# Kernel optimization log

Hardware: AMD Instinct MI355X
Metric: run time of the kernel (lower is better)

The kernel has to match this reference:

```python
import jax, jax.numpy as jnp
import numpy as np

N = 20000
E = 640000
IN_DIM = 128
HID = 128
OUT = 64


def setup_inputs() -> dict:
    key = jax.random.key(0)
    ks = jax.random.split(key, 16)
    s = 0.05
    inp = {
        'feat': jax.random.normal(ks[0], (N, IN_DIM), jnp.float32),
        'edge_index': jax.random.randint(ks[1], (2, E), 0, N, jnp.int64),
        # GCNConv params
        'W_gcn': jax.random.normal(ks[2], (IN_DIM, HID), jnp.float32) * s,
        'b_gcn': jnp.zeros((HID,), jnp.float32),
        # SAGEConv params (lin_l: aggregated neighbors w/ bias; lin_r: root, no bias)
        'W_sage_l': jax.random.normal(ks[3], (HID, HID), jnp.float32) * s,
        'b_sage_l': jnp.zeros((HID,), jnp.float32),
        'W_sage_r': jax.random.normal(ks[4], (HID, HID), jnp.float32) * s,
        # policy MLP
        'W1': jax.random.normal(ks[5], (HID, HID), jnp.float32) * s,
        'b1': jnp.zeros((HID,), jnp.float32),
        'W2': jax.random.normal(ks[6], (HID, HID), jnp.float32) * s,
        'b2': jnp.zeros((HID,), jnp.float32),
        'W3': jax.random.normal(ks[7], (HID, OUT), jnp.float32) * s,
        'b3': jnp.zeros((OUT,), jnp.float32),
        # value head
        'Wv': jax.random.normal(ks[8], (HID, 1), jnp.float32) * s,
        'bv': jnp.zeros((1,), jnp.float32),
    }
    return inp


def _gcn(feat, src, dst, W, b):
    # PyG GCNConv: add self loops, sym-normalize by deg^-1/2 on both ends
    loop = jnp.arange(N, dtype=src.dtype)
    s = jnp.concatenate([src, loop])
    d = jnp.concatenate([dst, loop])
    deg = jax.ops.segment_sum(jnp.ones_like(d, jnp.float32), d, num_segments=N)
    dinv = jnp.where(deg > 0, jax.lax.rsqrt(deg), 0.0)
    x = feat @ W  # [N, HID]
    msg = x[s] * (dinv[s] * dinv[d])[:, None]  # [E+N, HID]
    return jax.ops.segment_sum(msg, d, num_segments=N) + b


def _sage_mean(h, src, dst, Wl, bl, Wr):
    # PyG SAGEConv(aggr='mean'): lin_l(mean_neigh) + lin_r(root)
    neigh_sum = jax.ops.segment_sum(h[src], dst, num_segments=N)
    cnt = jax.ops.segment_sum(jnp.ones_like(dst, jnp.float32), dst, num_segments=N)
    mean = neigh_sum / jnp.maximum(cnt, 1.0)[:, None]
    return mean @ Wl + bl + h @ Wr


def reference(feat, edge_index, W_gcn, b_gcn, W_sage_l, b_sage_l, W_sage_r,
              W1, b1, W2, b2, W3, b3, Wv, bv):
    src, dst = edge_index[0], edge_index[1]
    h = jax.nn.relu(_gcn(feat, src, dst, W_gcn, b_gcn))
    h = jax.nn.relu(_sage_mean(h, src, dst, W_sage_l, b_sage_l, W_sage_r))
    # policy MLP (GELU exact, matching torch nn.GELU default)
    z = jax.nn.gelu(h @ W1 + b1, approximate=False)
    z = jax.nn.gelu(z @ W2 + b2, approximate=False)
    means = z @ W3 + b3  # [N, OUT]
    values = (h @ Wv + bv)[:, 0]  # [N]
    return (means, values)
```

## Files before the change

### kernel.cpp

```cpp
#include <hip/hip_runtime.h>
#include <math.h>


typedef __attribute__((ext_vector_type(8))) short short8;
typedef __attribute__((ext_vector_type(4))) float floatx4;

__device__ __forceinline__ unsigned short f2b(float f) {
    unsigned u = __float_as_uint(f);
    unsigned r = (u + 0x7fffu + ((u >> 16) & 1u)) >> 16;
    return (unsigned short)r;
}
__device__ __forceinline__ float b2f_lo(unsigned v) {
    return __uint_as_float(v << 16);
}
__device__ __forceinline__ float b2f_hi(unsigned v) {
    return __uint_as_float(v & 0xffff0000u);
}
__device__ __forceinline__ floatx4 MFMA(short8 a, short8 b, floatx4 c) {
    return __builtin_amdgcn_mfma_f32_16x16x32_bf16(a, b, c, 0, 0, 0);
}
__device__ __forceinline__ float gelu_exact(float x) {
    return 0.5f * x * (1.0f + erff(x * 0.70710678118654752440f));
}

#define FRAG(P, ct, ks, lane) (*(const short8*)((P) + (((((ct)*4 + (ks))*64) + (lane)) << 3)))


__global__ __launch_bounds__(256) void count_pack_kernel(
    const int* __restrict__ eidx, int E, int* __restrict__ cnt,
    const float* Wg, const float* Wsl, const float* Wsr,
    const float* W1, const float* W2, const float* W3,
    unsigned short* Pg, unsigned short* Psl, unsigned short* Psr,
    unsigned short* P1, unsigned short* P2, unsigned short* P3,
    int countBlocks)
{
    if ((int)blockIdx.x < countBlocks) {
        int e = blockIdx.x * 256 + threadIdx.x;
        if (e < E) atomicAdd(&cnt[eidx[E + e]], 1);
        return;
    }
    int t = (blockIdx.x - countBlocks) * 256 + threadIdx.x;
    const float* W; unsigned short* P; int NC = 128; int base;
    if (t < 2048)       { W = Wg;  P = Pg;  base = t; }
    else if (t < 4096)  { W = Wsl; P = Psl; base = t - 2048; }
    else if (t < 6144)  { W = Wsr; P = Psr; base = t - 4096; }
    else if (t < 8192)  { W = W1;  P = P1;  base = t - 6144; }
    else if (t < 10240) { W = W2;  P = P2;  base = t - 8192; }
    else if (t < 11264) { W = W3;  P = P3;  base = t - 10240; NC = 64; }
    else return;
    int l  = base & 63;
    int ks = (base >> 6) & 3;
    int ct = base >> 8;
    int n  = ct * 16 + (l & 15);
    int k0 = ks * 32 + ((l >> 4) << 3);
    short8 v;
    #pragma unroll
    for (int j = 0; j < 8; j++) v[j] = (short)f2b(W[(size_t)(k0 + j) * NC + n]);
    *(short8*)(P + ((size_t)base << 3)) = v;
}


__global__ __launch_bounds__(256) void scan_kernel(
    const int* __restrict__ cnt, int N,
    int* __restrict__ row_ptr, int* __restrict__ wptr, float* __restrict__ dinv,
    int* __restrict__ gflags, int* __restrict__ gsums)
{
    __shared__ int sh[256];
    __shared__ int s_off;
    int b = blockIdx.x, tid = threadIdx.x;
    int i0 = b * 1024 + tid * 4;
    int v0 = (i0 + 0 < N) ? cnt[i0 + 0] : 0;
    int v1 = (i0 + 1 < N) ? cnt[i0 + 1] : 0;
    int v2 = (i0 + 2 < N) ? cnt[i0 + 2] : 0;
    int v3 = (i0 + 3 < N) ? cnt[i0 + 3] : 0;
    int tot = v0 + v1 + v2 + v3;
    sh[tid] = tot;
    __syncthreads();
    for (int off = 1; off < 256; off <<= 1) {
        int t = (tid >= off) ? sh[tid - off] : 0;
        __syncthreads();
        sh[tid] += t;
        __syncthreads();
    }
    if (tid == 255) {
        gsums[b] = sh[255];
        __hip_atomic_store(&gflags[b], 1, __ATOMIC_RELEASE, __HIP_MEMORY_SCOPE_AGENT);
    }
    if (tid == 0) {
        int off = 0;
        for (int j = 0; j < b; j++) {
            while (__hip_atomic_load(&gflags[j], __ATOMIC_ACQUIRE,
                                     __HIP_MEMORY_SCOPE_AGENT) == 0) {}
            off += gsums[j];
        }
        s_off = off;
    }
    __syncthreads();
    int excl = s_off + sh[tid] - tot;
    if (i0 + 0 < N) { row_ptr[i0 + 0] = excl;                wptr[i0 + 0] = excl;                dinv[i0 + 0] = rsqrtf((float)(v0 + 1)); }
    if (i0 + 1 < N) { row_ptr[i0 + 1] = excl + v0;           wptr[i0 + 1] = excl + v0;           dinv[i0 + 1] = rsqrtf((float)(v1 + 1)); }
    if (i0 + 2 < N) { row_ptr[i0 + 2] = excl + v0 + v1;      wptr[i0 + 2] = excl + v0 + v1;      dinv[i0 + 2] = rsqrtf((float)(v2 + 1)); }
    if (i0 + 3 < N) { row_ptr[i0 + 3] = excl + v0 + v1 + v2; wptr[i0 + 3] = excl + v0 + v1 + v2; dinv[i0 + 3] = rsqrtf((float)(v3 + 1)); }
    if (b == (int)gridDim.x - 1 && tid == 255) row_ptr[N] = s_off + sh[255];
}


__global__ __launch_bounds__(256) void fill_gemm_kernel(
    const int* __restrict__ eidx, int E, int N,
    int* __restrict__ wptr, int* __restrict__ col,
    const float* __restrict__ feat, const float* __restrict__ dinv,
    const unsigned short* __restrict__ Pg, unsigned short* __restrict__ xs,
    int M, int fillBlocks, int PS)
{
    if ((int)blockIdx.x < fillBlocks) {
        int p = blockIdx.x & 7;
        int chunk = blockIdx.x >> 3;
        int dlo = p * PS;
        int dhi = dlo + PS; if (dhi > N) dhi = N;
        #pragma unroll
        for (int it = 0; it < 8; it++) {
            int e = (chunk * 8 + it) * 256 + threadIdx.x;
            if (e < E) {
                int d = eidx[E + e];
                if (d >= dlo && d < dhi) {
                    int pos = atomicAdd(&wptr[d], 1);
                    col[pos] = eidx[e];
                }
            }
        }
        return;
    }
    int bid = blockIdx.x - fillBlocks;
    int w = bid * 4 + (threadIdx.x >> 6);
    if (w >= (M / 16) * 2) return;
    int lane = threadIdx.x & 63;
    int m = lane & 15, quad = lane >> 4;
    int rt = w >> 1, ch = w & 1;
    const float* arow = feat + (size_t)(rt * 16 + m) * 128;
    short8 a[4];
    #pragma unroll
    for (int ks = 0; ks < 4; ks++) {
        float4 f0 = *(const float4*)(arow + ks * 32 + quad * 8);
        float4 f1 = *(const float4*)(arow + ks * 32 + quad * 8 + 4);
        short8 s;
        s[0] = (short)f2b(f0.x); s[1] = (short)f2b(f0.y);
        s[2] = (short)f2b(f0.z); s[3] = (short)f2b(f0.w);
        s[4] = (short)f2b(f1.x); s[5] = (short)f2b(f1.y);
        s[6] = (short)f2b(f1.z); s[7] = (short)f2b(f1.w);
        a[ks] = s;
    }
    float dvr[4];
    #pragma unroll
    for (int reg = 0; reg < 4; reg++) dvr[reg] = dinv[rt * 16 + quad * 4 + reg];
    #pragma unroll
    for (int ct = 0; ct < 4; ct++) {
        floatx4 acc = {0.f, 0.f, 0.f, 0.f};
        #pragma unroll
        for (int ks = 0; ks < 4; ks++)
            acc = MFMA(a[ks], FRAG(Pg, ch * 4 + ct, ks, lane), acc);
        #pragma unroll
        for (int reg = 0; reg < 4; reg++)
            xs[(size_t)(rt * 16 + quad * 4 + reg) * 128 + (ch * 4 + ct) * 16 + m] =
                f2b(acc[reg] * dvr[reg]);
    }
}


#define ACCUM(q)                                   \
    acc[0] += b2f_lo((q).x); acc[1] += b2f_hi((q).x); \
    acc[2] += b2f_lo((q).y); acc[3] += b2f_hi((q).y); \
    acc[4] += b2f_lo((q).z); acc[5] += b2f_hi((q).z); \
    acc[6] += b2f_lo((q).w); acc[7] += b2f_hi((q).w);

template<bool GCN>
__global__ __launch_bounds__(256) void agg_kernel(
    const unsigned short* __restrict__ X, const int* __restrict__ row_ptr,
    const int* __restrict__ col, const float* __restrict__ dinv,
    const float* __restrict__ bias, unsigned short* __restrict__ Y, int N)
{
    int w = (int)((blockIdx.x * 256 + threadIdx.x) >> 6);
    if (w >= N) return;
    int lane = threadIdx.x & 63;
    int g = lane >> 4, t = lane & 15;
    const uint4* Xq = (const uint4*)X;
    int beg = row_ptr[w], end = row_ptr[w + 1];
    int deg = end - beg;

    float acc[8] = {0.f, 0.f, 0.f, 0.f, 0.f, 0.f, 0.f, 0.f};
    int jb = beg;
    for (; jb + 16 <= end; jb += 16) {
        int s0 = col[jb + g];
        int s1 = col[jb + g + 4];
        int s2 = col[jb + g + 8];
        int s3 = col[jb + g + 12];
        uint4 q0 = Xq[(size_t)s0 * 16 + t];
        uint4 q1 = Xq[(size_t)s1 * 16 + t];
        uint4 q2 = Xq[(size_t)s2 * 16 + t];
        uint4 q3 = Xq[(size_t)s3 * 16 + t];
        ACCUM(q0) ACCUM(q1) ACCUM(q2) ACCUM(q3)
    }
    for (; jb < end; jb += 4) {
        int j = jb + g;
        if (j < end) {
            int s = col[j];
            uint4 q = Xq[(size_t)s * 16 + t];
            ACCUM(q)
        }
    }
    #pragma unroll
    for (int i = 0; i < 8; i++) {
        acc[i] += __shfl_xor(acc[i], 16);
        acc[i] += __shfl_xor(acc[i], 32);
    }
    if (g == 0) {
        float out[8];
        if (GCN) {
            uint4 q = Xq[(size_t)w * 16 + t];
            ACCUM(q)
            float dw = dinv[w];
            float4 b0 = *(const float4*)(bias + t * 8);
            float4 b1 = *(const float4*)(bias + t * 8 + 4);
            out[0] = fmaxf(fmaf(acc[0], dw, b0.x), 0.f);
            out[1] = fmaxf(fmaf(acc[1], dw, b0.y), 0.f);
            out[2] = fmaxf(fmaf(acc[2], dw, b0.z), 0.f);
            out[3] = fmaxf(fmaf(acc[3], dw, b0.w), 0.f);
            out[4] = fmaxf(fmaf(acc[4], dw, b1.x), 0.f);
            out[5] = fmaxf(fmaf(acc[5], dw, b1.y), 0.f);
            out[6] = fmaxf(fmaf(acc[6], dw, b1.z), 0.f);
            out[7] = fmaxf(fmaf(acc[7], dw, b1.w), 0.f);
        } else {
            float rc = 1.0f / (float)(deg > 0 ? deg : 1);
            #pragma unroll
            for (int i = 0; i < 8; i++) out[i] = acc[i] * rc;
        }
        uint4 r;
        r.x = (unsigned)f2b(out[0]) | ((unsigned)f2b(out[1]) << 16);
        r.y = (unsigned)f2b(out[2]) | ((unsigned)f2b(out[3]) << 16);
        r.z = (unsigned)f2b(out[4]) | ((unsigned)f2b(out[5]) << 16);
        r.w = (unsigned)f2b(out[6]) | ((unsigned)f2b(out[7]) << 16);
        ((uint4*)Y)[(size_t)w * 16 + t] = r;
    }
}


__global__ __launch_bounds__(256) void sage_mlp_kernel(
    const unsigned short* __restrict__ mean, const unsigned short* __restrict__ h1,
    const unsigned short* __restrict__ Psl, const unsigned short* __restrict__ Psr,
    const float* __restrict__ bsl,
    const unsigned short* __restrict__ P1, const float* __restrict__ b1,
    const unsigned short* __restrict__ P2, const float* __restrict__ b2,
    const unsigned short* __restrict__ P3, const float* __restrict__ b3,
    const float* __restrict__ Wv, const float* __restrict__ bv,
    float* __restrict__ means, float* __restrict__ values, int M)
{
    __shared__ unsigned short z[4][16 * 136];
    int widx = threadIdx.x >> 6, lane = threadIdx.x & 63;
    int w = blockIdx.x * 4 + widx;
    if (w >= M / 16) return;
    int m = lane & 15, quad = lane >> 4;
    unsigned short* zt = &z[widx][0];
    int r0 = w * 16;

    short8 am[4], ar[4];
    #pragma unroll
    for (int ks = 0; ks < 4; ks++) {
        am[ks] = *(const short8*)(mean + (size_t)(r0 + m) * 128 + ks * 32 + quad * 8);
        ar[ks] = *(const short8*)(h1   + (size_t)(r0 + m) * 128 + ks * 32 + quad * 8);
    }

    float vpart[4] = {0.f, 0.f, 0.f, 0.f};
    #pragma unroll
    for (int ct = 0; ct < 8; ct++) {
        floatx4 acc = {0.f, 0.f, 0.f, 0.f};
        #pragma unroll
        for (int ks = 0; ks < 4; ks++) acc = MFMA(am[ks], FRAG(Psl, ct, ks, lane), acc);
        #pragma unroll
        for (int ks = 0; ks < 4; ks++) acc = MFMA(ar[ks], FRAG(Psr, ct, ks, lane), acc);
        float bb = bsl[ct * 16 + m];
        float wv = Wv[ct * 16 + m];
        #pragma unroll
        for (int reg = 0; reg < 4; reg++) {
            float o = fmaxf(acc[reg] + bb, 0.f);
            vpart[reg] = fmaf(o, wv, vpart[reg]);
            zt[(quad * 4 + reg) * 136 + ct * 16 + m] = f2b(o);
        }
    }
    #pragma unroll
    for (int off = 1; off <= 8; off <<= 1) {
        #pragma unroll
        for (int reg = 0; reg < 4; reg++)
            vpart[reg] += __shfl_xor(vpart[reg], off);
    }
    if (m == 0) {
        float bvv = bv[0];
        #pragma unroll
        for (int reg = 0; reg < 4; reg++)
            values[r0 + quad * 4 + reg] = vpart[reg] + bvv;
    }

    short8 a1[4];
    #pragma unroll
    for (int ks = 0; ks < 4; ks++)
        a1[ks] = *(const short8*)(zt + m * 136 + ks * 32 + quad * 8);

    #pragma unroll
    for (int ct = 0; ct < 8; ct++) {
        floatx4 acc = {0.f, 0.f, 0.f, 0.f};
        #pragma unroll
        for (int ks = 0; ks < 4; ks++) acc = MFMA(a1[ks], FRAG(P1, ct, ks, lane), acc);
        float bb = b1[ct * 16 + m];
        #pragma unroll
        for (int reg = 0; reg < 4; reg++)
            zt[(quad * 4 + reg) * 136 + ct * 16 + m] = f2b(gelu_exact(acc[reg] + bb));
    }
    short8 a2[4];
    #pragma unroll
    for (int ks = 0; ks < 4; ks++)
        a2[ks] = *(const short8*)(zt + m * 136 + ks * 32 + quad * 8);

    #pragma unroll
    for (int ct = 0; ct < 8; ct++) {
        floatx4 acc = {0.f, 0.f, 0.f, 0.f};
        #pragma unroll
        for (int ks = 0; ks < 4; ks++) acc = MFMA(a2[ks], FRAG(P2, ct, ks, lane), acc);
        float bb = b2[ct * 16 + m];
        #pragma unroll
        for (int reg = 0; reg < 4; reg++)
            zt[(quad * 4 + reg) * 136 + ct * 16 + m] = f2b(gelu_exact(acc[reg] + bb));
    }
    short8 a3[4];
    #pragma unroll
    for (int ks = 0; ks < 4; ks++)
        a3[ks] = *(const short8*)(zt + m * 136 + ks * 32 + quad * 8);

    #pragma unroll
    for (int ct = 0; ct < 4; ct++) {
        floatx4 acc = {0.f, 0.f, 0.f, 0.f};
        #pragma unroll
        for (int ks = 0; ks < 4; ks++) acc = MFMA(a3[ks], FRAG(P3, ct, ks, lane), acc);
        float bb = b3[ct * 16 + m];
        #pragma unroll
        for (int reg = 0; reg < 4; reg++)
            means[(size_t)(r0 + quad * 4 + reg) * 64 + ct * 16 + m] = acc[reg] + bb;
    }
}


extern "C" void kernel_launch(void* const* d_in, const int* in_sizes, int n_in,
                              void* d_out, int out_size, void* d_ws, size_t ws_size,
                              hipStream_t stream) {
    const float* feat  = (const float*)d_in[0];
    const int*   eidx  = (const int*)d_in[1];
    const float* W_gcn = (const float*)d_in[2];
    const float* b_gcn = (const float*)d_in[3];
    const float* W_sl  = (const float*)d_in[4];
    const float* b_sl  = (const float*)d_in[5];
    const float* W_sr  = (const float*)d_in[6];
    const float* W1    = (const float*)d_in[7];
    const float* b1    = (const float*)d_in[8];
    const float* W2    = (const float*)d_in[9];
    const float* b2    = (const float*)d_in[10];
    const float* W3    = (const float*)d_in[11];
    const float* b3    = (const float*)d_in[12];
    const float* Wv    = (const float*)d_in[13];
    const float* bv    = (const float*)d_in[14];

    const int N = in_sizes[0] / 128;
    const int E = in_sizes[1] / 2;

    char* ws = (char*)d_ws;
    size_t off = 0;
    auto alloc = [&](size_t bytes) -> void* {
        void* p = ws + off;
        off += (bytes + 255) & ~(size_t)255;
        return p;
    };
    int*   gflags  = (int*)alloc((size_t)(64 + N) * 4);
    int*   cnt     = gflags + 64;
    size_t zbytes  = (size_t)(64 + N) * 4;
    int*   gsums   = (int*)alloc(64 * 4);
    int*   row_ptr = (int*)alloc((size_t)(N + 1) * 4);
    int*   wptr    = (int*)alloc((size_t)N * 4);
    float* dinv    = (float*)alloc((size_t)N * 4);
    int*   col     = (int*)alloc((size_t)E * 4);
    unsigned short* xs   = (unsigned short*)alloc((size_t)N * 128 * 2);
    unsigned short* h1   = (unsigned short*)alloc((size_t)N * 128 * 2);
    unsigned short* mean = (unsigned short*)alloc((size_t)N * 128 * 2);
    unsigned short* Pg   = (unsigned short*)alloc(2048 * 8 * 2);
    unsigned short* Psl  = (unsigned short*)alloc(2048 * 8 * 2);
    unsigned short* Psr  = (unsigned short*)alloc(2048 * 8 * 2);
    unsigned short* P1   = (unsigned short*)alloc(2048 * 8 * 2);
    unsigned short* P2   = (unsigned short*)alloc(2048 * 8 * 2);
    unsigned short* P3   = (unsigned short*)alloc(1024 * 8 * 2);

    hipMemsetAsync(gflags, 0, zbytes, stream);

    const int countBlocks = (E + 255) / 256;
    const int packBlocks  = (11264 + 255) / 256;
    count_pack_kernel<<<countBlocks + packBlocks, 256, 0, stream>>>(
        eidx, E, cnt, W_gcn, W_sl, W_sr, W1, W2, W3,
        Pg, Psl, Psr, P1, P2, P3, countBlocks);

    const int NB = (N + 1023) / 1024;
    scan_kernel<<<NB, 256, 0, stream>>>(cnt, N, row_ptr, wptr, dinv, gflags, gsums);

    const int PS = (N + 7) / 8;
    const int chunks = (E + 2047) / 2048;
    const int fillBlocks = chunks * 8;
    const int gemmBlocks = ((N / 16) * 2 + 3) / 4;
    fill_gemm_kernel<<<fillBlocks + gemmBlocks, 256, 0, stream>>>(
        eidx, E, N, wptr, col, feat, dinv, Pg, xs, N, fillBlocks, PS);

    const int agrid = (N + 3) / 4;
    agg_kernel<true><<<agrid, 256, 0, stream>>>(xs, row_ptr, col, dinv, b_gcn, h1, N);
    agg_kernel<false><<<agrid, 256, 0, stream>>>(h1, row_ptr, col, dinv, nullptr, mean, N);

    sage_mlp_kernel<<<(N / 16 + 3) / 4, 256, 0, stream>>>(
        mean, h1, Psl, Psr, b_sl, P1, b1, P2, b2, P3, b3, Wv, bv,
        (float*)d_out, (float*)d_out + (size_t)N * 64, N);
}
```

Measured before the change: 221.0 us.

## Fuse all GNN stages into one persistent kernel with grid barriers

Replaces the five separate kernels (count/pack, scan, fill+GEMM, two aggregations, SAGE+MLP) with a single persistent mega-kernel of 240 blocks of 512 threads that moves between phases through atomic grid-wide barriers. CSR fill now appears to use a per-edge rank array instead of a partitioned atomic cursor. The aggregation also processes two destination rows per wave at once to raise memory-level parallelism. This removes kernel launch gaps and tail effects. In exchange it relies on all blocks being co-resident for the spin barriers, and it caps parallelism at a fixed grid.

```diff
diff --git a/kernel.cpp b/kernel.cpp
--- a/kernel.cpp
+++ b/kernel.cpp
@@ -7,47 +7,36 @@
 
 __device__ __forceinline__ unsigned short f2b(float f) {
     unsigned u = __float_as_uint(f);
-    unsigned r = (u + 0x7fffu + ((u >> 16) & 1u)) >> 16;
-    return (unsigned short)r;
-}
-__device__ __forceinline__ float b2f_lo(unsigned v) {
-    return __uint_as_float(v << 16);
-}
-__device__ __forceinline__ float b2f_hi(unsigned v) {
-    return __uint_as_float(v & 0xffff0000u);
-}
+    return (unsigned short)((u + 0x7fffu + ((u >> 16) & 1u)) >> 16);
+}
+__device__ __forceinline__ unsigned pack2(float a, float b) {
+    return (unsigned)f2b(a) | ((unsigned)f2b(b) << 16);
+}
+__device__ __forceinline__ float b2f_lo(unsigned v) { return __uint_as_float(v << 16); }
+__device__ __forceinline__ float b2f_hi(unsigned v) { return __uint_as_float(v & 0xffff0000u); }
 __device__ __forceinline__ floatx4 MFMA(short8 a, short8 b, floatx4 c) {
     return __builtin_amdgcn_mfma_f32_16x16x32_bf16(a, b, c, 0, 0, 0);
 }
 __device__ __forceinline__ float gelu_exact(float x) {
     return 0.5f * x * (1.0f + erff(x * 0.70710678118654752440f));
 }
-
 #define FRAG(P, ct, ks, lane) (*(const short8*)((P) + (((((ct)*4 + (ks))*64) + (lane)) << 3)))
 
-
-__global__ __launch_bounds__(256) void count_pack_kernel(
-    const int* __restrict__ eidx, int E, int* __restrict__ cnt,
-    const float* Wg, const float* Wsl, const float* Wsr,
-    const float* W1, const float* W2, const float* W3,
-    unsigned short* Pg, unsigned short* Psl, unsigned short* Psr,
-    unsigned short* P1, unsigned short* P2, unsigned short* P3,
-    int countBlocks)
-{
-    if ((int)blockIdx.x < countBlocks) {
-        int e = blockIdx.x * 256 + threadIdx.x;
-        if (e < E) atomicAdd(&cnt[eidx[E + e]], 1);
-        return;
-    }
-    int t = (blockIdx.x - countBlocks) * 256 + threadIdx.x;
-    const float* W; unsigned short* P; int NC = 128; int base;
-    if (t < 2048)       { W = Wg;  P = Pg;  base = t; }
-    else if (t < 4096)  { W = Wsl; P = Psl; base = t - 2048; }
-    else if (t < 6144)  { W = Wsr; P = Psr; base = t - 4096; }
-    else if (t < 8192)  { W = W1;  P = P1;  base = t - 6144; }
-    else if (t < 10240) { W = W2;  P = P2;  base = t - 8192; }
-    else if (t < 11264) { W = W3;  P = P3;  base = t - 10240; NC = 64; }
-    else return;
+__device__ __forceinline__ void gbar(int* bar, int slot, int nblk) {
+    __syncthreads();
+    if (threadIdx.x == 0) {
+        __threadfence();
+        __hip_atomic_fetch_add(&bar[slot * 32], 1, __ATOMIC_RELEASE,
+                               __HIP_MEMORY_SCOPE_AGENT);
+        while (__hip_atomic_load(&bar[slot * 32], __ATOMIC_ACQUIRE,
+                                 __HIP_MEMORY_SCOPE_AGENT) < nblk) {
+            __builtin_amdgcn_s_sleep(1);
+        }
+    }
+    __syncthreads();
+}
+
+__device__ __forceinline__ void pack_one(const float* W, unsigned short* P, int NC, int base) {
     int l  = base & 63;
     int ks = (base >> 6) & 3;
     int ct = base >> 8;
@@ -59,289 +48,300 @@
     *(short8*)(P + ((size_t)base << 3)) = v;
 }
 
-
-__global__ __launch_bounds__(256) void scan_kernel(
-    const int* __restrict__ cnt, int N,
-    int* __restrict__ row_ptr, int* __restrict__ wptr, float* __restrict__ dinv,
-    int* __restrict__ gflags, int* __restrict__ gsums)
+__device__ __forceinline__ void accum8(float* acc, uint4 q) {
+    acc[0] += b2f_lo(q.x); acc[1] += b2f_hi(q.x);
+    acc[2] += b2f_lo(q.y); acc[3] += b2f_hi(q.y);
+    acc[4] += b2f_lo(q.z); acc[5] += b2f_hi(q.z);
+    acc[6] += b2f_lo(q.w); acc[7] += b2f_hi(q.w);
+}
+__device__ __forceinline__ void step16(const uint4* Xq, const int* __restrict__ col,
+                                       int jb, int g, int t, float* acc) {
+    int s0 = col[jb + g];
+    int s1 = col[jb + 4 + g];
+    int s2 = col[jb + 8 + g];
+    int s3 = col[jb + 12 + g];
+    uint4 q0 = Xq[(size_t)s0 * 16 + t];
+    uint4 q1 = Xq[(size_t)s1 * 16 + t];
+    uint4 q2 = Xq[(size_t)s2 * 16 + t];
+    uint4 q3 = Xq[(size_t)s3 * 16 + t];
+    accum8(acc, q0); accum8(acc, q1); accum8(acc, q2); accum8(acc, q3);
+}
+__device__ __forceinline__ void tail4(const uint4* Xq, const int* __restrict__ col,
+                                      int jb, int end, int g, int t, float* acc) {
+    for (int j = jb + g; j < end; j += 4) {
+        int s = col[j];
+        uint4 q = Xq[(size_t)s * 16 + t];
+        accum8(acc, q);
+    }
+}
+__device__ __forceinline__ void store_gcn(unsigned short* Y, const uint4* Xq,
+                                          const float* dinv, const float* bias,
+                                          int w, int t, float* acc) {
+    uint4 q = Xq[(size_t)w * 16 + t];
+    accum8(acc, q);
+    float dw = dinv[w];
+    float4 b0 = *(const float4*)(bias + t * 8);
+    float4 b1 = *(const float4*)(bias + t * 8 + 4);
+    uint4 r;
+    r.x = pack2(fmaxf(fmaf(acc[0], dw, b0.x), 0.f), fmaxf(fmaf(acc[1], dw, b0.y), 0.f));
+    r.y = pack2(fmaxf(fmaf(acc[2], dw, b0.z), 0.f), fmaxf(fmaf(acc[3], dw, b0.w), 0.f));
+    r.z = pack2(fmaxf(fmaf(acc[4], dw, b1.x), 0.f), fmaxf(fmaf(acc[5], dw, b1.y), 0.f));
+    r.w = pack2(fmaxf(fmaf(acc[6], dw, b1.z), 0.f), fmaxf(fmaf(acc[7], dw, b1.w), 0.f));
+    ((uint4*)Y)[(size_t)w * 16 + t] = r;
+}
+__device__ __forceinline__ void store_mean(unsigned short* Y, int w, int t, int deg, float* acc) {
+    float rc = 1.0f / (float)(deg > 0 ? deg : 1);
+    uint4 r;
+    r.x = pack2(acc[0] * rc, acc[1] * rc);
+    r.y = pack2(acc[2] * rc, acc[3] * rc);
+    r.z = pack2(acc[4] * rc, acc[5] * rc);
+    r.w = pack2(acc[6] * rc, acc[7] * rc);
+    ((uint4*)Y)[(size_t)w * 16 + t] = r;
+}
+
+__device__ void agg_phase(bool gcn, const unsigned short* X, const int* __restrict__ row_ptr,
+                          const int* __restrict__ col, const float* __restrict__ dinv,
+                          const float* __restrict__ bias, unsigned short* Y,
+                          int N, int wi, int nw, int lane)
 {
-    __shared__ int sh[256];
-    __shared__ int s_off;
-    int b = blockIdx.x, tid = threadIdx.x;
-    int i0 = b * 1024 + tid * 4;
-    int v0 = (i0 + 0 < N) ? cnt[i0 + 0] : 0;
-    int v1 = (i0 + 1 < N) ? cnt[i0 + 1] : 0;
-    int v2 = (i0 + 2 < N) ? cnt[i0 + 2] : 0;
-    int v3 = (i0 + 3 < N) ? cnt[i0 + 3] : 0;
-    int tot = v0 + v1 + v2 + v3;
-    sh[tid] = tot;
-    __syncthreads();
-    for (int off = 1; off < 256; off <<= 1) {
-        int t = (tid >= off) ? sh[tid - off] : 0;
-        __syncthreads();
-        sh[tid] += t;
-        __syncthreads();
-    }
-    if (tid == 255) {
-        gsums[b] = sh[255];
-        __hip_atomic_store(&gflags[b], 1, __ATOMIC_RELEASE, __HIP_MEMORY_SCOPE_AGENT);
-    }
-    if (tid == 0) {
-        int off = 0;
-        for (int j = 0; j < b; j++) {
-            while (__hip_atomic_load(&gflags[j], __ATOMIC_ACQUIRE,
-                                     __HIP_MEMORY_SCOPE_AGENT) == 0) {}
-            off += gsums[j];
-        }
-        s_off = off;
-    }
-    __syncthreads();
-    int excl = s_off + sh[tid] - tot;
-    if (i0 + 0 < N) { row_ptr[i0 + 0] = excl;                wptr[i0 + 0] = excl;                dinv[i0 + 0] = rsqrtf((float)(v0 + 1)); }
-    if (i0 + 1 < N) { row_ptr[i0 + 1] = excl + v0;           wptr[i0 + 1] = excl + v0;           dinv[i0 + 1] = rsqrtf((float)(v1 + 1)); }
-    if (i0 + 2 < N) { row_ptr[i0 + 2] = excl + v0 + v1;      wptr[i0 + 2] = excl + v0 + v1;      dinv[i0 + 2] = rsqrtf((float)(v2 + 1)); }
-    if (i0 + 3 < N) { row_ptr[i0 + 3] = excl + v0 + v1 + v2; wptr[i0 + 3] = excl + v0 + v1 + v2; dinv[i0 + 3] = rsqrtf((float)(v3 + 1)); }
-    if (b == (int)gridDim.x - 1 && tid == 255) row_ptr[N] = s_off + sh[255];
-}
-
-
-__global__ __launch_bounds__(256) void fill_gemm_kernel(
-    const int* __restrict__ eidx, int E, int N,
-    int* __restrict__ wptr, int* __restrict__ col,
-    const float* __restrict__ feat, const float* __restrict__ dinv,
-    const unsigned short* __restrict__ Pg, unsigned short* __restrict__ xs,
-    int M, int fillBlocks, int PS)
-{
-    if ((int)blockIdx.x < fillBlocks) {
-        int p = blockIdx.x & 7;
-        int chunk = blockIdx.x >> 3;
-        int dlo = p * PS;
-        int dhi = dlo + PS; if (dhi > N) dhi = N;
-        #pragma unroll
-        for (int it = 0; it < 8; it++) {
-            int e = (chunk * 8 + it) * 256 + threadIdx.x;
-            if (e < E) {
-                int d = eidx[E + e];
-                if (d >= dlo && d < dhi) {
-                    int pos = atomicAdd(&wptr[d], 1);
-                    col[pos] = eidx[e];
-                }
-            }
-        }
-        return;
-    }
-    int bid = blockIdx.x - fillBlocks;
-    int w = bid * 4 + (threadIdx.x >> 6);
-    if (w >= (M / 16) * 2) return;
-    int lane = threadIdx.x & 63;
-    int m = lane & 15, quad = lane >> 4;
-    int rt = w >> 1, ch = w & 1;
-    const float* arow = feat + (size_t)(rt * 16 + m) * 128;
-    short8 a[4];
-    #pragma unroll
-    for (int ks = 0; ks < 4; ks++) {
-        float4 f0 = *(const float4*)(arow + ks * 32 + quad * 8);
-        float4 f1 = *(const float4*)(arow + ks * 32 + quad * 8 + 4);
-        short8 s;
-        s[0] = (short)f2b(f0.x); s[1] = (short)f2b(f0.y);
-        s[2] = (short)f2b(f0.z); s[3] = (short)f2b(f0.w);
-        s[4] = (short)f2b(f1.x); s[5] = (short)f2b(f1.y);
-        s[6] = (short)f2b(f1.z); s[7] = (short)f2b(f1.w);
-        a[ks] = s;
-    }
-    float dvr[4];
-    #pragma unroll
-    for (int reg = 0; reg < 4; reg++) dvr[reg] = dinv[rt * 16 + quad * 4 + reg];
-    #pragma unroll
-    for (int ct = 0; ct < 4; ct++) {
-        floatx4 acc = {0.f, 0.f, 0.f, 0.f};
-        #pragma unroll
-        for (int ks = 0; ks < 4; ks++)
-            acc = MFMA(a[ks], FRAG(Pg, ch * 4 + ct, ks, lane), acc);
-        #pragma unroll
-        for (int reg = 0; reg < 4; reg++)
-            xs[(size_t)(rt * 16 + quad * 4 + reg) * 128 + (ch * 4 + ct) * 16 + m] =
-                f2b(acc[reg] * dvr[reg]);
-    }
-}
-
-
-#define ACCUM(q)                                   \
-    acc[0] += b2f_lo((q).x); acc[1] += b2f_hi((q).x); \
-    acc[2] += b2f_lo((q).y); acc[3] += b2f_hi((q).y); \
-    acc[4] += b2f_lo((q).z); acc[5] += b2f_hi((q).z); \
-    acc[6] += b2f_lo((q).w); acc[7] += b2f_hi((q).w);
-
-template<bool GCN>
-__global__ __launch_bounds__(256) void agg_kernel(
-    const unsigned short* __restrict__ X, const int* __restrict__ row_ptr,
-    const int* __restrict__ col, const float* __restrict__ dinv,
-    const float* __restrict__ bias, unsigned short* __restrict__ Y, int N)
-{
-    int w = (int)((blockIdx.x * 256 + threadIdx.x) >> 6);
-    if (w >= N) return;
-    int lane = threadIdx.x & 63;
     int g = lane >> 4, t = lane & 15;
     const uint4* Xq = (const uint4*)X;
-    int beg = row_ptr[w], end = row_ptr[w + 1];
-    int deg = end - beg;
-
-    float acc[8] = {0.f, 0.f, 0.f, 0.f, 0.f, 0.f, 0.f, 0.f};
-    int jb = beg;
-    for (; jb + 16 <= end; jb += 16) {
-        int s0 = col[jb + g];
-        int s1 = col[jb + g + 4];
-        int s2 = col[jb + g + 8];
-        int s3 = col[jb + g + 12];
-        uint4 q0 = Xq[(size_t)s0 * 16 + t];
-        uint4 q1 = Xq[(size_t)s1 * 16 + t];
-        uint4 q2 = Xq[(size_t)s2 * 16 + t];
-        uint4 q3 = Xq[(size_t)s3 * 16 + t];
-        ACCUM(q0) ACCUM(q1) ACCUM(q2) ACCUM(q3)
-    }
-    for (; jb < end; jb += 4) {
-        int j = jb + g;
-        if (j < end) {
-            int s = col[j];
-            uint4 q = Xq[(size_t)s * 16 + t];
-            ACCUM(q)
-        }
-    }
-    #pragma unroll
-    for (int i = 0; i < 8; i++) {
-        acc[i] += __shfl_xor(acc[i], 16);
-        acc[i] += __shfl_xor(acc[i], 32);
-    }
-    if (g == 0) {
-        float out[8];
-        if (GCN) {
-            uint4 q = Xq[(size_t)w * 16 + t];
-            ACCUM(q)
-            float dw = dinv[w];
-            float4 b0 = *(const float4*)(bias + t * 8);
-            float4 b1 = *(const float4*)(bias + t * 8 + 4);
-            out[0] = fmaxf(fmaf(acc[0], dw, b0.x), 0.f);
-            out[1] = fmaxf(fmaf(acc[1], dw, b0.y), 0.f);
-            out[2] = fmaxf(fmaf(acc[2], dw, b0.z), 0.f);
-            out[3] = fmaxf(fmaf(acc[3], dw, b0.w), 0.f);
-            out[4] = fmaxf(fmaf(acc[4], dw, b1.x), 0.f);
-            out[5] = fmaxf(fmaf(acc[5], dw, b1.y), 0.f);
-            out[6] = fmaxf(fmaf(acc[6], dw, b1.z), 0.f);
-            out[7] = fmaxf(fmaf(acc[7], dw, b1.w), 0.f);
+    for (int pw = wi; pw * 2 < N; pw += nw) {
+        int w0 = pw * 2, w1 = w0 + 1;
+        int beg0 = row_ptr[w0];
+        int mid  = row_ptr[w1];
+        int end1 = row_ptr[w1 + 1];
+        float acc0[8] = {0.f,0.f,0.f,0.f,0.f,0.f,0.f,0.f};
+        float acc1[8] = {0.f,0.f,0.f,0.f,0.f,0.f,0.f,0.f};
+        int jb0 = beg0, jb1 = mid;
+        while (jb0 + 16 <= mid && jb1 + 16 <= end1) {
+            step16(Xq, col, jb0, g, t, acc0);
+            step16(Xq, col, jb1, g, t, acc1);
+            jb0 += 16; jb1 += 16;
+        }
+        while (jb0 + 16 <= mid)  { step16(Xq, col, jb0, g, t, acc0); jb0 += 16; }
+        while (jb1 + 16 <= end1) { step16(Xq, col, jb1, g, t, acc1); jb1 += 16; }
+        tail4(Xq, col, jb0, mid,  g, t, acc0);
+        tail4(Xq, col, jb1, end1, g, t, acc1);
+        #pragma unroll
+        for (int i = 0; i < 8; i++) {
+            acc0[i] += __shfl_xor(acc0[i], 16); acc0[i] += __shfl_xor(acc0[i], 32);
+            acc1[i] += __shfl_xor(acc1[i], 16); acc1[i] += __shfl_xor(acc1[i], 32);
+        }
+        if (gcn) {
+            if (g == 0)      store_gcn(Y, Xq, dinv, bias, w0, t, acc0);
+            else if (g == 1) store_gcn(Y, Xq, dinv, bias, w1, t, acc1);
         } else {
-            float rc = 1.0f / (float)(deg > 0 ? deg : 1);
-            #pragma unroll
-            for (int i = 0; i < 8; i++) out[i] = acc[i] * rc;
-        }
-        uint4 r;
-        r.x = (unsigned)f2b(out[0]) | ((unsigned)f2b(out[1]) << 16);
-        r.y = (unsigned)f2b(out[2]) | ((unsigned)f2b(out[3]) << 16);
-        r.z = (unsigned)f2b(out[4]) | ((unsigned)f2b(out[5]) << 16);
-        r.w = (unsigned)f2b(out[6]) | ((unsigned)f2b(out[7]) << 16);
-        ((uint4*)Y)[(size_t)w * 16 + t] = r;
-    }
-}
-
-
-__global__ __launch_bounds__(256) void sage_mlp_kernel(
-    const unsigned short* __restrict__ mean, const unsigned short* __restrict__ h1,
-    const unsigned short* __restrict__ Psl, const unsigned short* __restrict__ Psr,
-    const float* __restrict__ bsl,
-    const unsigned short* __restrict__ P1, const float* __restrict__ b1,
-    const unsigned short* __restrict__ P2, const float* __restrict__ b2,
-    const unsigned short* __restrict__ P3, const float* __restrict__ b3,
-    const float* __restrict__ Wv, const float* __restrict__ bv,
-    float* __restrict__ means, float* __restrict__ values, int M)
+            if (g == 0)      store_mean(Y, w0, t, mid - beg0, acc0);
+            else if (g == 1) store_mean(Y, w1, t, end1 - mid, acc1);
+        }
+    }
+}
+
+__global__ __launch_bounds__(512, 2) void mega_kernel(
+    const float* __restrict__ feat, const int* __restrict__ eidx,
+    const float* __restrict__ Wg,  const float* __restrict__ bg,
+    const float* __restrict__ Wsl, const float* __restrict__ bsl,
+    const float* __restrict__ Wsr,
+    const float* __restrict__ W1,  const float* __restrict__ b1,
+    const float* __restrict__ W2,  const float* __restrict__ b2,
+    const float* __restrict__ W3,  const float* __restrict__ b3,
+    const float* __restrict__ Wv,  const float* __restrict__ bv,
+    int* bar, int* cnt, int* rank, int* row_ptr, float* dinv, int* col, int* gsums,
+    unsigned short* xs, unsigned short* h1, unsigned short* mean,
+    unsigned short* Pg, unsigned short* Psl, unsigned short* Psr,
+    unsigned short* P1p, unsigned short* P2p, unsigned short* P3p,
+    float* means, float* values, int N, int E)
 {
-    __shared__ unsigned short z[4][16 * 136];
-    int widx = threadIdx.x >> 6, lane = threadIdx.x & 63;
-    int w = blockIdx.x * 4 + widx;
-    if (w >= M / 16) return;
-    int m = lane & 15, quad = lane >> 4;
-    unsigned short* zt = &z[widx][0];
-    int r0 = w * 16;
-
-    short8 am[4], ar[4];
-    #pragma unroll
-    for (int ks = 0; ks < 4; ks++) {
-        am[ks] = *(const short8*)(mean + (size_t)(r0 + m) * 128 + ks * 32 + quad * 8);
-        ar[ks] = *(const short8*)(h1   + (size_t)(r0 + m) * 128 + ks * 32 + quad * 8);
-    }
-
-    float vpart[4] = {0.f, 0.f, 0.f, 0.f};
-    #pragma unroll
-    for (int ct = 0; ct < 8; ct++) {
-        floatx4 acc = {0.f, 0.f, 0.f, 0.f};
-        #pragma unroll
-        for (int ks = 0; ks < 4; ks++) acc = MFMA(am[ks], FRAG(Psl, ct, ks, lane), acc);
-        #pragma unroll
-        for (int ks = 0; ks < 4; ks++) acc = MFMA(ar[ks], FRAG(Psr, ct, ks, lane), acc);
-        float bb = bsl[ct * 16 + m];
-        float wv = Wv[ct * 16 + m];
-        #pragma unroll
-        for (int reg = 0; reg < 4; reg++) {
-            float o = fmaxf(acc[reg] + bb, 0.f);
-            vpart[reg] = fmaf(o, wv, vpart[reg]);
-            zt[(quad * 4 + reg) * 136 + ct * 16 + m] = f2b(o);
-        }
-    }
-    #pragma unroll
-    for (int off = 1; off <= 8; off <<= 1) {
-        #pragma unroll
-        for (int reg = 0; reg < 4; reg++)
-            vpart[reg] += __shfl_xor(vpart[reg], off);
-    }
-    if (m == 0) {
-        float bvv = bv[0];
-        #pragma unroll
-        for (int reg = 0; reg < 4; reg++)
-            values[r0 + quad * 4 + reg] = vpart[reg] + bvv;
-    }
-
-    short8 a1[4];
-    #pragma unroll
-    for (int ks = 0; ks < 4; ks++)
-        a1[ks] = *(const short8*)(zt + m * 136 + ks * 32 + quad * 8);
-
-    #pragma unroll
-    for (int ct = 0; ct < 8; ct++) {
-        floatx4 acc = {0.f, 0.f, 0.f, 0.f};
-        #pragma unroll
-        for (int ks = 0; ks < 4; ks++) acc = MFMA(a1[ks], FRAG(P1, ct, ks, lane), acc);
-        float bb = b1[ct * 16 + m];
-        #pragma unroll
-        for (int reg = 0; reg < 4; reg++)
-            zt[(quad * 4 + reg) * 136 + ct * 16 + m] = f2b(gelu_exact(acc[reg] + bb));
-    }
-    short8 a2[4];
-    #pragma unroll
-    for (int ks = 0; ks < 4; ks++)
-        a2[ks] = *(const short8*)(zt + m * 136 + ks * 32 + quad * 8);
-
-    #pragma unroll
-    for (int ct = 0; ct < 8; ct++) {
-        floatx4 acc = {0.f, 0.f, 0.f, 0.f};
-        #pragma unroll
-        for (int ks = 0; ks < 4; ks++) acc = MFMA(a2[ks], FRAG(P2, ct, ks, lane), acc);
-        float bb = b2[ct * 16 + m];
-        #pragma unroll
-        for (int reg = 0; reg < 4; reg++)
-            zt[(quad * 4 + reg) * 136 + ct * 16 + m] = f2b(gelu_exact(acc[reg] + bb));
-    }
-    short8 a3[4];
-    #pragma unroll
-    for (int ks = 0; ks < 4; ks++)
-        a3[ks] = *(const short8*)(zt + m * 136 + ks * 32 + quad * 8);
-
-    #pragma unroll
-    for (int ct = 0; ct < 4; ct++) {
-        floatx4 acc = {0.f, 0.f, 0.f, 0.f};
-        #pragma unroll
-        for (int ks = 0; ks < 4; ks++) acc = MFMA(a3[ks], FRAG(P3, ct, ks, lane), acc);
-        float bb = b3[ct * 16 + m];
-        #pragma unroll
-        for (int reg = 0; reg < 4; reg++)
-            means[(size_t)(r0 + quad * 4 + reg) * 64 + ct * 16 + m] = acc[reg] + bb;
+    const int tid  = threadIdx.x;
+    const int nblk = gridDim.x;
+    const int gtid = blockIdx.x * 512 + tid;
+    const int GT   = nblk * 512;
+    const int lane = tid & 63;
+    const int widx = tid >> 6;
+    const int wi   = gtid >> 6;
+    const int nw   = GT >> 6;
+
+    __shared__ union { int gs[256]; unsigned short mlp[8 * 2176]; } sm;
+    __shared__ int loc[96];
+    __shared__ int red[512];
+
+    for (int t0 = gtid; t0 < 11264; t0 += GT) {
+        if      (t0 < 2048)  pack_one(Wg,  Pg,  128, t0);
+        else if (t0 < 4096)  pack_one(Wsl, Psl, 128, t0 - 2048);
+        else if (t0 < 6144)  pack_one(Wsr, Psr, 128, t0 - 4096);
+        else if (t0 < 8192)  pack_one(W1,  P1p, 128, t0 - 6144);
+        else if (t0 < 10240) pack_one(W2,  P2p, 128, t0 - 8192);
+        else                 pack_one(W3,  P3p, 64,  t0 - 10240);
+    }
+    gbar(bar, 0, nblk);
+
+    for (int e = gtid; e < E; e += GT)
+        rank[e] = atomicAdd(&cnt[eidx[E + e]], 1);
+    gbar(bar, 1, nblk);
+
+    const int NPB = (N + nblk - 1) / nblk;
+    const int n0  = blockIdx.x * NPB;
+    int ncount = N - n0; if (ncount > NPB) ncount = NPB; if (ncount < 0) ncount = 0;
+    if (tid < ncount) loc[tid] = cnt[n0 + tid];
+    __syncthreads();
+    if (tid == 0) {
+        int s = 0;
+        for (int i = 0; i < ncount; i++) { int v = loc[i]; loc[i] = s; s += v; }
+        gsums[blockIdx.x] = s;
+    }
+    gbar(bar, 2, nblk);
+
+    for (int i = tid; i < nblk; i += 512) sm.gs[i] = gsums[i];
+    __syncthreads();
+    {
+        int p = 0;
+        for (int j = tid; j < (int)blockIdx.x; j += 512) p += sm.gs[j];
+        red[tid] = p;
+        __syncthreads();
+        for (int s = 256; s > 0; s >>= 1) {
+            if (tid < s) red[tid] += red[tid + s];
+            __syncthreads();
+        }
+    }
+    const int boff = red[0];
+    for (int i = tid; i < ncount; i += 512) {
+        row_ptr[n0 + i] = boff + loc[i];
+        dinv[n0 + i] = rsqrtf((float)(cnt[n0 + i] + 1));
+    }
+    if (gtid == 0) row_ptr[N] = E;
+    gbar(bar, 3, nblk);
+
+    for (int e = gtid; e < E; e += GT) {
+        int d = eidx[E + e];
+        col[row_ptr[d] + rank[e]] = eidx[e];
+    }
+    {
+        const int m = lane & 15, quad = lane >> 4;
+        const int T2 = (N / 16) * 2;
+        for (int w = wi; w < T2; w += nw) {
+            int rt = w >> 1, ch = w & 1;
+            const float* arow = feat + (size_t)(rt * 16 + m) * 128;
+            short8 a[4];
+            #pragma unroll
+            for (int ks = 0; ks < 4; ks++) {
+                float4 f0 = *(const float4*)(arow + ks * 32 + quad * 8);
+                float4 f1 = *(const float4*)(arow + ks * 32 + quad * 8 + 4);
+                short8 s;
+                s[0] = (short)f2b(f0.x); s[1] = (short)f2b(f0.y);
+                s[2] = (short)f2b(f0.z); s[3] = (short)f2b(f0.w);
+                s[4] = (short)f2b(f1.x); s[5] = (short)f2b(f1.y);
+                s[6] = (short)f2b(f1.z); s[7] = (short)f2b(f1.w);
+                a[ks] = s;
+            }
+            float dvr[4];
+            #pragma unroll
+            for (int reg = 0; reg < 4; reg++) dvr[reg] = dinv[rt * 16 + quad * 4 + reg];
+            #pragma unroll
+            for (int ct = 0; ct < 4; ct++) {
+                floatx4 acc = {0.f, 0.f, 0.f, 0.f};
+                #pragma unroll
+                for (int ks = 0; ks < 4; ks++)
+                    acc = MFMA(a[ks], FRAG(Pg, ch * 4 + ct, ks, lane), acc);
+                #pragma unroll
+                for (int reg = 0; reg < 4; reg++)
+                    xs[(size_t)(rt * 16 + quad * 4 + reg) * 128 + (ch * 4 + ct) * 16 + m] =
+                        f2b(acc[reg] * dvr[reg]);
+            }
+        }
+    }
+    gbar(bar, 4, nblk);
+
+    agg_phase(true, xs, row_ptr, col, dinv, bg, h1, N, wi, nw, lane);
+    gbar(bar, 5, nblk);
+
+    agg_phase(false, h1, row_ptr, col, dinv, nullptr, mean, N, wi, nw, lane);
+    gbar(bar, 6, nblk);
+
+    {
+        unsigned short* zt = &sm.mlp[widx * 2176];
+        const int m = lane & 15, quad = lane >> 4;
+        const int M16 = N / 16;
+        for (int w = wi; w < M16; w += nw) {
+            int r0 = w * 16;
+            short8 am[4], ar[4];
+            #pragma unroll
+            for (int ks = 0; ks < 4; ks++) {
+                am[ks] = *(const short8*)(mean + (size_t)(r0 + m) * 128 + ks * 32 + quad * 8);
+                ar[ks] = *(const short8*)(h1   + (size_t)(r0 + m) * 128 + ks * 32 + quad * 8);
+            }
+            float vpart[4] = {0.f, 0.f, 0.f, 0.f};
+            #pragma unroll
+            for (int ct = 0; ct < 8; ct++) {
+                floatx4 acc = {0.f, 0.f, 0.f, 0.f};
+                #pragma unroll
+                for (int ks = 0; ks < 4; ks++) acc = MFMA(am[ks], FRAG(Psl, ct, ks, lane), acc);
+                #pragma unroll
+                for (int ks = 0; ks < 4; ks++) acc = MFMA(ar[ks], FRAG(Psr, ct, ks, lane), acc);
+                float bb = bsl[ct * 16 + m];
+                float wv = Wv[ct * 16 + m];
+                #pragma unroll
+                for (int reg = 0; reg < 4; reg++) {
+                    float o = fmaxf(acc[reg] + bb, 0.f);
+                    vpart[reg] = fmaf(o, wv, vpart[reg]);
+                    zt[(quad * 4 + reg) * 136 + ct * 16 + m] = f2b(o);
+                }
+            }
+            #pragma unroll
+            for (int off = 1; off <= 8; off <<= 1) {
+                #pragma unroll
+                for (int reg = 0; reg < 4; reg++)
+                    vpart[reg] += __shfl_xor(vpart[reg], off);
+            }
+            if (m == 0) {
+                float bvv = bv[0];
+                #pragma unroll
+                for (int reg = 0; reg < 4; reg++)
+                    values[r0 + quad * 4 + reg] = vpart[reg] + bvv;
+            }
+            short8 a1[4];
+            #pragma unroll
+            for (int ks = 0; ks < 4; ks++)
+                a1[ks] = *(const short8*)(zt + m * 136 + ks * 32 + quad * 8);
+            #pragma unroll
+            for (int ct = 0; ct < 8; ct++) {
+                floatx4 acc = {0.f, 0.f, 0.f, 0.f};
+                #pragma unroll
+                for (int ks = 0; ks < 4; ks++) acc = MFMA(a1[ks], FRAG(P1p, ct, ks, lane), acc);
+                float bb = b1[ct * 16 + m];
+                #pragma unroll
+                for (int reg = 0; reg < 4; reg++)
+                    zt[(quad * 4 + reg) * 136 + ct * 16 + m] = f2b(gelu_exact(acc[reg] + bb));
+            }
+            short8 a2[4];
+            #pragma unroll
+            for (int ks = 0; ks < 4; ks++)
+                a2[ks] = *(const short8*)(zt + m * 136 + ks * 32 + quad * 8);
+            #pragma unroll
+            for (int ct = 0; ct < 8; ct++) {
+                floatx4 acc = {0.f, 0.f, 0.f, 0.f};
+                #pragma unroll
+                for (int ks = 0; ks < 4; ks++) acc = MFMA(a2[ks], FRAG(P2p, ct, ks, lane), acc);
+                float bb = b2[ct * 16 + m];
+                #pragma unroll
+                for (int reg = 0; reg < 4; reg++)
+                    zt[(quad * 4 + reg) * 136 + ct * 16 + m] = f2b(gelu_exact(acc[reg] + bb));
+            }
+            short8 a3[4];
+            #pragma unroll
+            for (int ks = 0; ks < 4; ks++)
+                a3[ks] = *(const short8*)(zt + m * 136 + ks * 32 + quad * 8);
+            #pragma unroll
+            for (int ct = 0; ct < 4; ct++) {
+                floatx4 acc = {0.f, 0.f, 0.f, 0.f};
+                #pragma unroll
+                for (int ks = 0; ks < 4; ks++) acc = MFMA(a3[ks], FRAG(P3p, ct, ks, lane), acc);
+                float bb = b3[ct * 16 + m];
+                #pragma unroll
+                for (int reg = 0; reg < 4; reg++)
+                    means[(size_t)(r0 + quad * 4 + reg) * 64 + ct * 16 + m] = acc[reg] + bb;
+            }
+        }
     }
 }
 
@@ -365,8 +365,8 @@
     const float* Wv    = (const float*)d_in[13];
     const float* bv    = (const float*)d_in[14];
 
-    const int N = in_sizes[0] / 128;
-    const int E = in_sizes[1] / 2;
+    int N = in_sizes[0] / 128;
+    int E = in_sizes[1] / 2;
 
     char* ws = (char*)d_ws;
     size_t off = 0;
@@ -375,47 +375,33 @@
         off += (bytes + 255) & ~(size_t)255;
         return p;
     };
-    int*   gflags  = (int*)alloc((size_t)(64 + N) * 4);
-    int*   cnt     = gflags + 64;
-    size_t zbytes  = (size_t)(64 + N) * 4;
-    int*   gsums   = (int*)alloc(64 * 4);
+    int*   bar     = (int*)alloc((size_t)(512 + N) * 4);
+    int*   cnt     = bar + 512;
+    size_t zbytes  = (size_t)(512 + N) * 4;
+    int*   rank    = (int*)alloc((size_t)E * 4);
     int*   row_ptr = (int*)alloc((size_t)(N + 1) * 4);
-    int*   wptr    = (int*)alloc((size_t)N * 4);
     float* dinv    = (float*)alloc((size_t)N * 4);
     int*   col     = (int*)alloc((size_t)E * 4);
+    int*   gsums   = (int*)alloc(256 * 4);
     unsigned short* xs   = (unsigned short*)alloc((size_t)N * 128 * 2);
     unsigned short* h1   = (unsigned short*)alloc((size_t)N * 128 * 2);
     unsigned short* mean = (unsigned short*)alloc((size_t)N * 128 * 2);
     unsigned short* Pg   = (unsigned short*)alloc(2048 * 8 * 2);
     unsigned short* Psl  = (unsigned short*)alloc(2048 * 8 * 2);
     unsigned short* Psr  = (unsigned short*)alloc(2048 * 8 * 2);
-    unsigned short* P1   = (unsigned short*)alloc(2048 * 8 * 2);
-    unsigned short* P2   = (unsigned short*)alloc(2048 * 8 * 2);
-    unsigned short* P3   = (unsigned short*)alloc(1024 * 8 * 2);
-
-    hipMemsetAsync(gflags, 0, zbytes, stream);
-
-    const int countBlocks = (E + 255) / 256;
-    const int packBlocks  = (11264 + 255) / 256;
-    count_pack_kernel<<<countBlocks + packBlocks, 256, 0, stream>>>(
-        eidx, E, cnt, W_gcn, W_sl, W_sr, W1, W2, W3,
-        Pg, Psl, Psr, P1, P2, P3, countBlocks);
-
-    const int NB = (N + 1023) / 1024;
-    scan_kernel<<<NB, 256, 0, stream>>>(cnt, N, row_ptr, wptr, dinv, gflags, gsums);
-
-    const int PS = (N + 7) / 8;
-    const int chunks = (E + 2047) / 2048;
-    const int fillBlocks = chunks * 8;
-    const int gemmBlocks = ((N / 16) * 2 + 3) / 4;
-    fill_gemm_kernel<<<fillBlocks + gemmBlocks, 256, 0, stream>>>(
-        eidx, E, N, wptr, col, feat, dinv, Pg, xs, N, fillBlocks, PS);
-
-    const int agrid = (N + 3) / 4;
-    agg_kernel<true><<<agrid, 256, 0, stream>>>(xs, row_ptr, col, dinv, b_gcn, h1, N);
-    agg_kernel<false><<<agrid, 256, 0, stream>>>(h1, row_ptr, col, dinv, nullptr, mean, N);
-
-    sage_mlp_kernel<<<(N / 16 + 3) / 4, 256, 0, stream>>>(
-        mean, h1, Psl, Psr, b_sl, P1, b1, P2, b2, P3, b3, Wv, bv,
-        (float*)d_out, (float*)d_out + (size_t)N * 64, N);
-}
+    unsigned short* P1p  = (unsigned short*)alloc(2048 * 8 * 2);
+    unsigned short* P2p  = (unsigned short*)alloc(2048 * 8 * 2);
+    unsigned short* P3p  = (unsigned short*)alloc(1024 * 8 * 2);
+
+    float* means  = (float*)d_out;
+    float* values = (float*)d_out + (size_t)N * 64;
+
+    hipMemsetAsync(bar, 0, zbytes, stream);
+
+    mega_kernel<<<240, 512, 0, stream>>>(
+        feat, eidx, W_gcn, b_gcn, W_sl, b_sl, W_sr,
+        W1, b1, W2, b2, W3, b3, Wv, bv,
+        bar, cnt, rank, row_ptr, dinv, col, gsums,
+        xs, h1, mean, Pg, Psl, Psr, P1p, P2p, P3p,
+        means, values, N, E);
+}
```

After: 451.4 us. 2.04x slower.
